# Optimization experiments

Hardware: AMD Instinct MI355X
Metric: run time of the kernel (lower is better)

## Reference

```python
import jax, jax.numpy as jnp
import numpy as np

EPS = 1e-6  # flax LayerNorm default
ROPE_BASE = 10000.0

def _ln(x, scale, bias):
    m = jnp.mean(x, axis=-1, keepdims=True)
    v = jnp.mean(jnp.square(x - m), axis=-1, keepdims=True)
    return (x - m) * jax.lax.rsqrt(v + EPS) * scale + bias

def _rope_cache(u, v, head_dim):
    # P = head_dim//2//2 pairs per axis
    P = head_dim // 4
    freqs = jnp.arange(P, dtype=jnp.float32) / (P - 1 + 1e-9)
    inv = 1.0 / ROPE_BASE ** freqs
    ang_x = jnp.einsum('nl,f->nlf', u, inv)
    ang_y = jnp.einsum('nl,f->nlf', v, inv)
    return jnp.cos(ang_x), jnp.sin(ang_x), jnp.cos(ang_y), jnp.sin(ang_y)

def _rope_apply(q, cos_x, sin_x, cos_y, sin_y):
    n, L, H, D = q.shape
    q = q.reshape(n, L, H, D // 2, 2)
    P = D // 4
    qx, qy = q[..., :P, :], q[..., P:, :]
    def rot(qp, c, s):
        c = c[:, :, None, :]
        s = s[:, :, None, :]
        x, y = qp[..., 0], qp[..., 1]
        return jnp.stack([x * c - y * s, x * s + y * c], axis=-1)
    return jnp.concatenate([rot(qx, cos_x, sin_x), rot(qy, cos_y, sin_y)], axis=-2).reshape(n, L, H, D)

def setup_inputs():
    key = jax.random.key(0)
    ks = jax.random.split(key, 12)
    N, HW, CIN = 8, 384, 3
    P, W, DPT, H, HD, MLP = 16, 768, 4, 12, 64, 3072
    s = 0.02
    return {
        'image': jax.random.normal(ks[0], (N, HW, HW, CIN), jnp.float32),
        'conv_kernel': jax.random.normal(ks[1], (P, P, CIN, W), jnp.float32) * s,
        'conv_bias': jnp.zeros((W,), jnp.float32),
        'ln1_scale': jnp.ones((DPT, W), jnp.float32),
        'ln1_bias': jnp.zeros((DPT, W), jnp.float32),
        'wq': jax.random.normal(ks[2], (DPT, W, H, HD), jnp.float32) * s,
        'bq': jnp.zeros((DPT, H, HD), jnp.float32),
        'wk': jax.random.normal(ks[3], (DPT, W, H, HD), jnp.float32) * s,
        'bk': jnp.zeros((DPT, H, HD), jnp.float32),
        'wv': jax.random.normal(ks[4], (DPT, W, H, HD), jnp.float32) * s,
        'bv': jnp.zeros((DPT, H, HD), jnp.float32),
        'wo': jax.random.normal(ks[5], (DPT, H, HD, W), jnp.float32) * s,
        'bo': jnp.zeros((DPT, W), jnp.float32),
        'ln2_scale': jnp.ones((DPT, W), jnp.float32),
        'ln2_bias': jnp.zeros((DPT, W), jnp.float32),
        'w1': jax.random.normal(ks[6], (DPT, W, MLP), jnp.float32) * s,
        'b1': jnp.zeros((DPT, MLP), jnp.float32),
        'w2': jax.random.normal(ks[7], (DPT, MLP, W), jnp.float32) * s,
        'b2': jnp.zeros((DPT, W), jnp.float32),
        'lnf_scale': jnp.ones((W,), jnp.float32),
        'lnf_bias': jnp.zeros((W,), jnp.float32),
    }

def reference(image, conv_kernel, conv_bias, ln1_scale, ln1_bias,
              wq, bq, wk, bk, wv, bv, wo, bo,
              ln2_scale, ln2_bias, w1, b1, w2, b2, lnf_scale, lnf_bias):
    patch = conv_kernel.shape[0]
    # patch-embedding conv, stride=patch, VALID padding (NHWC/HWIO)
    x = jax.lax.conv_general_dilated(
        image, conv_kernel, window_strides=(patch, patch), padding='VALID',
        dimension_numbers=('NHWC', 'HWIO', 'NHWC')) + conv_bias
    n, h, w, c = x.shape
    L = h * w
    x = x.reshape(n, L, c)

    depth, _, H, HD = wq.shape
    # RoPE 2D coordinates for square grid (default path when rope_uv is None)
    ys, xs = jnp.mgrid[:h, :w]
    u = jnp.tile(((xs.reshape(-1) + 0.5) / w)[None, :], [n, 1])
    v = jnp.tile(((ys.reshape(-1) + 0.5) / h)[None, :], [n, 1])
    cos_x, sin_x, cos_y, sin_y = _rope_cache(u, v, HD)

    scale = 1.0 / jnp.sqrt(jnp.float32(HD))
    for l in range(depth):
        y = _ln(x, ln1_scale[l], ln1_bias[l])
        q = jnp.einsum('nld,dhk->nlhk', y, wq[l]) + bq[l]
        k = jnp.einsum('nld,dhk->nlhk', y, wk[l]) + bk[l]
        vv = jnp.einsum('nld,dhk->nlhk', y, wv[l]) + bv[l]
        q = _rope_apply(q, cos_x, sin_x, cos_y, sin_y)
        k = _rope_apply(k, cos_x, sin_x, cos_y, sin_y)
        logits = jnp.einsum('nqhd,nkhd->nhqk', q, k) * scale
        attn = jax.nn.softmax(logits, axis=-1)
        o = jnp.einsum('nhqk,nkhd->nqhd', attn, vv)
        y = jnp.einsum('nqhd,hdo->nqo', o, wo[l]) + bo[l]
        x = x + y
        y = _ln(x, ln2_scale[l], ln2_bias[l])
        y = jax.nn.gelu(jnp.einsum('nld,df->nlf', y, w1[l]) + b1[l])
        y = jnp.einsum('nlf,fd->nld', y, w2[l]) + b2[l]
        x = x + y

    x = _ln(x, lnf_scale, lnf_bias)  # encoder_norm
    return jnp.mean(x, axis=1)       # gap pooling -> [n, width]
```

## Files before the change

kernel.cpp:

```cpp
#include <hip/hip_runtime.h>
#include <hip/hip_bf16.h>

typedef __hip_bfloat16 bf16;
typedef __bf16 bf16x8 __attribute__((ext_vector_type(8)));
typedef float f32x4  __attribute__((ext_vector_type(4)));

#define NBATCH 8
#define LTOK   576
#define NT     4608
#define CW     768
#define NH     12
#define HDIM   64
#define DEPTH  4
#define MLPW   3072
#define GRIDP  24
#define IMGS   384
#define QKVW   2304

static __device__ __forceinline__ unsigned bfpair(float a, float b){
    bf16 x = __float2bfloat16(a), y = __float2bfloat16(b);
    return ((unsigned)*(unsigned short*)&y << 16) | *(unsigned short*)&x;
}
static __device__ __forceinline__ float b2f(bf16 v){ return __bfloat162float(v); }

static __device__ __forceinline__ int xcd_swizzle(int orig, int nwg){
    int q = nwg >> 3, r = nwg & 7;
    int xcd = orig & 7, j = orig >> 3;
    int base = (xcd < r) ? xcd*(q+1) : r*(q+1) + (xcd-r)*q;
    return base + j;
}

static __device__ __forceinline__ void gl_lds16(const bf16* g, bf16* l){
    __builtin_amdgcn_global_load_lds(
        (const __attribute__((address_space(1))) unsigned int*)(const void*)g,
        (__attribute__((address_space(3))) unsigned int*)(void*)l, 16, 0, 0);
}

__global__ void rope_cache_kernel(float* __restrict__ rc){
    int idx = blockIdx.x*256 + threadIdx.x;
    if (idx >= LTOK*16) return;
    int l = idx >> 4, f = idx & 15;
    int py = l / GRIDP, px = l % GRIDP;
    float u = (px + 0.5f) / (float)GRIDP;
    float v = (py + 0.5f) / (float)GRIDP;
    float fr = (float)f / (15.0f + 1e-9f);
    float inv = expf(-fr * 9.210340371976184f);
    float sx, cx, sy, cy;
    sincosf(u * inv, &sx, &cx);
    sincosf(v * inv, &sy, &cy);
    rc[idx]         = cx;
    rc[idx + 9216]  = sx;
    rc[idx + 18432] = cy;
    rc[idx + 27648] = sy;
}

__global__ void patch_gather(const float* __restrict__ img, bf16* __restrict__ p){
    int idx = blockIdx.x*256 + threadIdx.x;
    int t = idx / CW, kk = idx % CW;
    int n = t / LTOK, l = t % LTOK;
    int py = l / GRIDP, px = l % GRIDP;
    int i = kk / 48, r = kk % 48, j = r / 3, c = r % 3;
    p[idx] = __float2bfloat16(img[((size_t)(n*IMGS + py*16 + i)*IMGS + px*16 + j)*3 + c]);
}

__global__ __launch_bounds__(256) void wtrans_b(const float* __restrict__ in, bf16* __restrict__ out,
                                                int K, int N, size_t inStride, size_t outStride){
    in  += blockIdx.z * inStride;
    out += blockIdx.z * outStride;
    __shared__ float t[32][33];
    const int n0 = blockIdx.x*32, k0 = blockIdx.y*32;
    const int tx = threadIdx.x & 31, ty = threadIdx.x >> 5;
    #pragma unroll
    for (int r = 0; r < 4; ++r)
        t[ty + 8*r][tx] = in[(size_t)(k0 + ty + 8*r)*N + n0 + tx];
    __syncthreads();
    #pragma unroll
    for (int r = 0; r < 4; ++r)
        out[(size_t)(n0 + ty + 8*r)*K + k0 + tx] = __float2bfloat16(t[tx][ty + 8*r]);
}

__global__ void bias_pack(const float* __restrict__ bq, const float* __restrict__ bk,
                          const float* __restrict__ bv, float* __restrict__ o){
    int idx = blockIdx.x*256 + threadIdx.x;
    int l = idx / QKVW, r = idx % QKVW;
    const float* src = (r < 768) ? (bq + l*768 + r) :
                       (r < 1536) ? (bk + l*768 + r - 768) : (bv + l*768 + r - 1536);
    o[idx] = *src;
}

static __device__ __forceinline__ float gelu_tanh(float x){
    float x3 = x*x*x;
    return 0.5f*x*(1.0f + tanhf(0.7978845608028654f*(x + 0.044715f*x3)));
}

template<int EPI, typename TC>
__global__ __launch_bounds__(256) void gemm_a(const bf16* __restrict__ A, int lda,
                                              const bf16* __restrict__ B, int ldb,
                                              const float* __restrict__ bias,
                                              TC* __restrict__ C, int ldc, int K){
    __shared__ bf16 As[2][128*64];
    __shared__ bf16 Bs[2][64*64];
    const int tid = threadIdx.x;
    const int w = tid >> 6, l = tid & 63;
    const int quad = l >> 4, lr = l & 15;
    const int wm = w & 1, wn = w >> 1;

    const int nwg = gridDim.x * gridDim.y;
    const int swz = xcd_swizzle(blockIdx.y * gridDim.x + blockIdx.x, nwg);
    const int rowT = (swz / gridDim.x) * 128;
    const int colT = (swz % gridDim.x) * 64;

    const int srow = l >> 3;
    const int schk = (l & 7) ^ (srow & 7);

    const bf16* Ap[4];
    const bf16* Bp[2];
    #pragma unroll
    for (int t = 0; t < 4; ++t)
        Ap[t] = A + (size_t)(rowT + (w*4+t)*8 + srow)*lda + schk*8;
    #pragma unroll
    for (int t = 0; t < 2; ++t)
        Bp[t] = B + (size_t)(colT + (w*2+t)*8 + srow)*ldb + schk*8;

    auto STAGE = [&](int k0, int buf){
        #pragma unroll
        for (int t = 0; t < 4; ++t) gl_lds16(Ap[t] + k0, &As[buf][(w*4+t)*512]);
        #pragma unroll
        for (int t = 0; t < 2; ++t) gl_lds16(Bp[t] + k0, &Bs[buf][(w*2+t)*512]);
    };

    f32x4 acc[4][2];
    #pragma unroll
    for (int i = 0; i < 4; ++i)
        #pragma unroll
        for (int j = 0; j < 2; ++j) acc[i][j] = (f32x4){0.f,0.f,0.f,0.f};

    const int S = K >> 6;
    STAGE(0, 0);
    if (S > 1) STAGE(64, 1);

    int cur = 0;
    for (int s = 0; s < S; ++s){
        if (s < S-1) asm volatile("s_waitcnt vmcnt(6)" ::: "memory");
        else         asm volatile("s_waitcnt vmcnt(0)" ::: "memory");
        __builtin_amdgcn_s_barrier();
        #pragma unroll
        for (int kh = 0; kh < 2; ++kh){
            bf16x8 af[4], bfr[2];
            #pragma unroll
            for (int i = 0; i < 4; ++i){
                int r = wm*64 + i*16 + lr;
                af[i] = *(const bf16x8*)(&As[cur][r*64 + (((kh*4 + quad) ^ (r & 7))*8)]);
            }
            #pragma unroll
            for (int j = 0; j < 2; ++j){
                int r = wn*32 + j*16 + lr;
                bfr[j] = *(const bf16x8*)(&Bs[cur][r*64 + (((kh*4 + quad) ^ (r & 7))*8)]);
            }
            #pragma unroll
            for (int i = 0; i < 4; ++i)
                #pragma unroll
                for (int j = 0; j < 2; ++j)
                    acc[i][j] = __builtin_amdgcn_mfma_f32_16x16x32_bf16(af[i], bfr[j], acc[i][j], 0, 0, 0);
        }
        __builtin_amdgcn_s_barrier();
        if (s + 2 < S) STAGE((s + 2)*64, cur);
        cur ^= 1;
    }

    #pragma unroll
    for (int i = 0; i < 4; ++i){
        #pragma unroll
        for (int j = 0; j < 2; ++j){
            const int row = rowT + wm*64 + i*16 + quad*4;
            const int col = colT + wn*32 + j*16 + lr;
            const float bb = bias ? bias[col] : 0.f;
            #pragma unroll
            for (int r = 0; r < 4; ++r){
                float val = acc[i][j][r] + bb;
                TC* cp = C + (size_t)(row + r)*ldc + col;
                if (EPI == 2) val = gelu_tanh(val);
                if (EPI == 1) val += *(float*)cp;
                if (EPI == 0 || EPI == 2) *(bf16*)cp = __float2bfloat16(val);
                else                      *(float*)cp = val;
            }
        }
    }
}

__global__ __launch_bounds__(256) void ln_wave(const float* __restrict__ x,
                                               const float* __restrict__ sc,
                                               const float* __restrict__ bs,
                                               bf16* __restrict__ y){
    const int tid = threadIdx.x, w = tid >> 6, l = tid & 63;
    const int t = blockIdx.x*4 + w;
    const float4* xr = (const float4*)(x + (size_t)t*CW);
    float4 a[3];
    #pragma unroll
    for (int i = 0; i < 3; ++i) a[i] = xr[l + 64*i];
    float s = 0.f;
    #pragma unroll
    for (int i = 0; i < 3; ++i) s += a[i].x + a[i].y + a[i].z + a[i].w;
    #pragma unroll
    for (int off = 1; off < 64; off <<= 1) s += __shfl_xor(s, off);
    const float m = s * (1.0f/768.0f);
    float vs = 0.f;
    #pragma unroll
    for (int i = 0; i < 3; ++i){
        float dx = a[i].x-m, dy = a[i].y-m, dz = a[i].z-m, dw = a[i].w-m;
        vs += dx*dx + dy*dy + dz*dz + dw*dw;
    }
    #pragma unroll
    for (int off = 1; off < 64; off <<= 1) vs += __shfl_xor(vs, off);
    const float rs = rsqrtf(vs*(1.0f/768.0f) + 1e-6f);
    const float4* scp = (const float4*)sc;
    const float4* bsp = (const float4*)bs;
    uint2* yr = (uint2*)(y + (size_t)t*CW);
    #pragma unroll
    for (int i = 0; i < 3; ++i){
        float4 sv = scp[l + 64*i], bv = bsp[l + 64*i];
        float r0 = (a[i].x-m)*rs*sv.x + bv.x;
        float r1 = (a[i].y-m)*rs*sv.y + bv.y;
        float r2 = (a[i].z-m)*rs*sv.z + bv.z;
        float r3 = (a[i].w-m)*rs*sv.w + bv.w;
        yr[l + 64*i] = make_uint2(bfpair(r0,r1), bfpair(r2,r3));
    }
}

__global__ void rope_qk(bf16* __restrict__ qkv, const float* __restrict__ rc){
    int idx = blockIdx.x*256 + threadIdx.x;
    int tok = idx / 768;
    int r = idx % 768;
    int rr, base;
    if (r < 384){ base = 0; rr = r; } else { base = 768; rr = r - 384; }
    int hh = rr >> 5, p = rr & 31;
    int l = tok % LTOK;
    float c, s;
    if (p < 16){ c = rc[l*16 + p];            s = rc[9216 + l*16 + p]; }
    else       { c = rc[18432 + l*16 + p-16]; s = rc[27648 + l*16 + p-16]; }
    bf16* pp = qkv + (size_t)tok*QKVW + base + hh*64 + 2*p;
    unsigned u = *(unsigned*)pp;
    bf16 lo = *(bf16*)&u; unsigned short hi16 = u >> 16; bf16 hi = *(bf16*)&hi16;
    float x = b2f(lo), y = b2f(hi);
    *(unsigned*)pp = bfpair(x*c - y*s, x*s + y*c);
}

__global__ __launch_bounds__(256) void vtrans(const bf16* __restrict__ qkv, bf16* __restrict__ vT){
    __shared__ bf16 tile[64][72];
    const int t0 = blockIdx.x*64, hI = blockIdx.y, nI = blockIdx.z;
    const size_t base = ((size_t)nI*LTOK + t0)*QKVW + 1536 + hI*64;
    const int tid = threadIdx.x;
    #pragma unroll
    for (int i = 0; i < 2; ++i){
        int g = i*256 + tid, r = g >> 3, c = g & 7;
        *(uint4*)&tile[r][c*8] = *(const uint4*)(qkv + base + (size_t)r*QKVW + c*8);
    }
    __syncthreads();
    const size_t obase = ((size_t)(nI*NH + hI)*64)*576 + t0;
    #pragma unroll
    for (int i = 0; i < 2; ++i){
        int g = i*256 + tid, d = g >> 3, c = g & 7;
        bf16 tmp[8];
        #pragma unroll
        for (int j = 0; j < 8; ++j) tmp[j] = tile[c*8 + j][d];
        *(uint4*)(vT + obase + (size_t)d*576 + c*8) = *(uint4*)tmp;
    }
}

__global__ __launch_bounds__(256) void attn_flash(const bf16* __restrict__ qkv,
                                                  const bf16* __restrict__ vT,
                                                  bf16* __restrict__ o){
    __shared__ bf16 Ks[64*72];
    __shared__ bf16 Vs[64*72];
    __shared__ bf16 Ps[64*72];
    __shared__ float alph[64];
    __shared__ float lsum[64];
    const int tid = threadIdx.x;
    const int w = tid >> 6, l = tid & 63;
    const int quad = l >> 4, lr = l & 15;

    const int nwg = gridDim.x * gridDim.y * gridDim.z;
    const int orig = (blockIdx.z * gridDim.y + blockIdx.y) * gridDim.x + blockIdx.x;
    const int swz = xcd_swizzle(orig, nwg);
    const int q0 = (swz % gridDim.x) * 64;
    const int t2 = swz / gridDim.x;
    const int hI = t2 % gridDim.y;
    const int nI = t2 / gridDim.y;

    const size_t tokBase = (size_t)nI * LTOK;
    const int off = hI * 64;
    const size_t vbase = ((size_t)(nI*NH + hI)*64)*576;

    bf16x8 qf[2];
    #pragma unroll
    for (int kh = 0; kh < 2; ++kh)
        qf[kh] = *(const bf16x8*)(qkv + (tokBase + q0 + w*16 + lr)*QKVW + off + kh*32 + quad*8);

    f32x4 oacc[4];
    #pragma unroll
    for (int j = 0; j < 4; ++j) oacc[j] = (f32x4){0.f,0.f,0.f,0.f};
    float m_run = -3.0e38f, l_run = 0.f;

    for (int ch = 0; ch < 9; ++ch){
        __syncthreads();
        #pragma unroll
        for (int i = 0; i < 2; ++i){
            int g = i*256 + tid, r = g >> 3, c = g & 7;
            *(uint4*)(Ks + r*72 + c*8) =
                *(const uint4*)(qkv + (tokBase + ch*64 + r)*QKVW + 768 + off + c*8);
        }
        #pragma unroll
        for (int i = 0; i < 2; ++i){
            int g = i*256 + tid, d = g >> 3, c = g & 7;
            *(uint4*)(Vs + d*72 + c*8) = *(const uint4*)(vT + vbase + (size_t)d*576 + ch*64 + c*8);
        }
        __syncthreads();

        f32x4 st[4];
        #pragma unroll
        for (int t = 0; t < 4; ++t){
            st[t] = (f32x4){0.f,0.f,0.f,0.f};
            #pragma unroll
            for (int kh = 0; kh < 2; ++kh){
                bf16x8 kf = *(const bf16x8*)(Ks + (t*16 + lr)*72 + kh*32 + quad*8);
                st[t] = __builtin_amdgcn_mfma_f32_16x16x32_bf16(kf, qf[kh], st[t], 0, 0, 0);
            }
        }
        float lm = -3.0e38f;
        #pragma unroll
        for (int t = 0; t < 4; ++t)
            #pragma unroll
            for (int r = 0; r < 4; ++r){
                st[t][r] *= 0.125f;
                lm = fmaxf(lm, st[t][r]);
            }
        lm = fmaxf(lm, __shfl_xor(lm, 16));
        lm = fmaxf(lm, __shfl_xor(lm, 32));
        float mn = fmaxf(m_run, lm);
        float alpha = __expf(m_run - mn);
        m_run = mn;
        float ls = 0.f;
        #pragma unroll
        for (int t = 0; t < 4; ++t)
            #pragma unroll
            for (int r = 0; r < 4; ++r){
                float p = __expf(st[t][r] - mn);
                st[t][r] = p; ls += p;
            }
        ls += __shfl_xor(ls, 16);
        ls += __shfl_xor(ls, 32);
        l_run = l_run*alpha + ls;
        if ((tid & 48) == 0) alph[w*16 + lr] = alpha;
        #pragma unroll
        for (int t = 0; t < 4; ++t)
            #pragma unroll
            for (int r = 0; r < 4; ++r)
                Ps[(w*16 + lr)*72 + t*16 + quad*4 + r] = __float2bfloat16(st[t][r]);
        float af[4];
        #pragma unroll
        for (int r = 0; r < 4; ++r) af[r] = alph[w*16 + quad*4 + r];
        #pragma unroll
        for (int j = 0; j < 4; ++j)
            #pragma unroll
            for (int r = 0; r < 4; ++r) oacc[j][r] *= af[r];
        #pragma unroll
        for (int kh = 0; kh < 2; ++kh){
            bf16x8 pf = *(const bf16x8*)(Ps + (w*16 + lr)*72 + kh*32 + quad*8);
            #pragma unroll
            for (int j = 0; j < 4; ++j){
                bf16x8 vf = *(const bf16x8*)(Vs + (j*16 + lr)*72 + kh*32 + quad*8);
                oacc[j] = __builtin_amdgcn_mfma_f32_16x16x32_bf16(pf, vf, oacc[j], 0, 0, 0);
            }
        }
    }

    if ((tid & 48) == 0) lsum[w*16 + lr] = l_run;
    float linv[4];
    #pragma unroll
    for (int r = 0; r < 4; ++r) linv[r] = 1.0f / lsum[w*16 + quad*4 + r];
    #pragma unroll
    for (int j = 0; j < 4; ++j)
        #pragma unroll
        for (int r = 0; r < 4; ++r)
            o[(tokBase + q0 + w*16 + quad*4 + r)*CW + off + j*16 + lr] =
                __float2bfloat16(oacc[j][r] * linv[r]);
}

__global__ void mean_kernel(const bf16* __restrict__ y, float* __restrict__ out){
    int c = blockIdx.x*256 + threadIdx.x;
    int n = blockIdx.y;
    float s = 0.f;
    for (int l = 0; l < LTOK; ++l) s += b2f(y[((size_t)n*LTOK + l)*CW + c]);
    out[n*CW + c] = s * (1.0f/576.0f);
}

extern "C" void kernel_launch(void* const* d_in, const int* in_sizes, int n_in,
                              void* d_out, int out_size, void* d_ws, size_t ws_size,
                              hipStream_t stream){
    const float* image = (const float*)d_in[0];
    const float* convk = (const float*)d_in[1];
    const float* convb = (const float*)d_in[2];
    const float* ln1s  = (const float*)d_in[3];
    const float* ln1b  = (const float*)d_in[4];
    const float* wq    = (const float*)d_in[5];
    const float* bq    = (const float*)d_in[6];
    const float* wk    = (const float*)d_in[7];
    const float* bk    = (const float*)d_in[8];
    const float* wv    = (const float*)d_in[9];
    const float* bv    = (const float*)d_in[10];
    const float* wo    = (const float*)d_in[11];
    const float* bo    = (const float*)d_in[12];
    const float* ln2s  = (const float*)d_in[13];
    const float* ln2b  = (const float*)d_in[14];
    const float* w1    = (const float*)d_in[15];
    const float* b1    = (const float*)d_in[16];
    const float* w2    = (const float*)d_in[17];
    const float* b2    = (const float*)d_in[18];
    const float* lnfs  = (const float*)d_in[19];
    const float* lnfb  = (const float*)d_in[20];
    float* out = (float*)d_out;

    const size_t u = (size_t)NT*CW;
    float* ws    = (float*)d_ws;
    float* ropeC = ws;
    float* bqkvA = ws + 36864;
    float* x     = bqkvA + 4*QKVW;
    bf16*  y     = (bf16*)(x + u);
    bf16*  qkv   = y + u;
    bf16*  o     = qkv + (size_t)NT*QKVW;
    bf16*  h     = o + u;
    bf16*  vT    = h + (size_t)NT*MLPW;
    bf16*  convT = vT + u;
    bf16*  wqkvT = convT + 589824;
    bf16*  woT   = wqkvT + (size_t)4*QKVW*CW;
    bf16*  w1T   = woT + (size_t)4*CW*CW;
    bf16*  w2T   = w1T + (size_t)4*CW*MLPW;

    rope_cache_kernel<<<36, 256, 0, stream>>>(ropeC);
    patch_gather<<<(NT*CW)/256, 256, 0, stream>>>(image, y);
    bias_pack<<<36, 256, 0, stream>>>(bq, bk, bv, bqkvA);
    wtrans_b<<<dim3(24,24,1), 256, 0, stream>>>(convk, convT, CW, CW, 0, 0);
    wtrans_b<<<dim3(24,24,4), 256, 0, stream>>>(wq, wqkvT,           CW, CW, (size_t)CW*CW, (size_t)QKVW*CW);
    wtrans_b<<<dim3(24,24,4), 256, 0, stream>>>(wk, wqkvT + 589824,  CW, CW, (size_t)CW*CW, (size_t)QKVW*CW);
    wtrans_b<<<dim3(24,24,4), 256, 0, stream>>>(wv, wqkvT + 1179648, CW, CW, (size_t)CW*CW, (size_t)QKVW*CW);
    wtrans_b<<<dim3(24,24,4), 256, 0, stream>>>(wo, woT,             CW, CW, (size_t)CW*CW, (size_t)CW*CW);
    wtrans_b<<<dim3(96,24,4), 256, 0, stream>>>(w1, w1T,  CW, MLPW, (size_t)CW*MLPW, (size_t)CW*MLPW);
    wtrans_b<<<dim3(24,96,4), 256, 0, stream>>>(w2, w2T, MLPW,  CW, (size_t)CW*MLPW, (size_t)CW*MLPW);

    gemm_a<3,float><<<dim3(12,36), 256, 0, stream>>>(y, CW, convT, CW, convb, x, CW, CW);

    for (int l = 0; l < DEPTH; ++l){
        ln_wave<<<NT/4, 256, 0, stream>>>(x, ln1s + l*CW, ln1b + l*CW, y);
        gemm_a<0,bf16><<<dim3(36,36), 256, 0, stream>>>(y, CW, wqkvT + (size_t)l*QKVW*CW, CW,
                                                        bqkvA + l*QKVW, qkv, QKVW, CW);
        rope_qk<<<(NT*768)/256, 256, 0, stream>>>(qkv, ropeC);
        vtrans<<<dim3(9, NH, NBATCH), 256, 0, stream>>>(qkv, vT);
        attn_flash<<<dim3(9, NH, NBATCH), 256, 0, stream>>>(qkv, vT, o);
        gemm_a<1,float><<<dim3(12,36), 256, 0, stream>>>(o, CW, woT + (size_t)l*CW*CW, CW,
                                                         bo + l*CW, x, CW, CW);
        ln_wave<<<NT/4, 256, 0, stream>>>(x, ln2s + l*CW, ln2b + l*CW, y);
        gemm_a<2,bf16><<<dim3(48,36), 256, 0, stream>>>(y, CW, w1T + (size_t)l*CW*MLPW, CW,
                                                        b1 + l*MLPW, h, MLPW, CW);
        gemm_a<1,float><<<dim3(12,36), 256, 0, stream>>>(h, MLPW, w2T + (size_t)l*CW*MLPW, MLPW,
                                                         b2 + l*CW, x, CW, MLPW);
    }
    ln_wave<<<NT/4, 256, 0, stream>>>(x, lnfs, lnfb, y);
    mean_kernel<<<dim3(3, NBATCH), 256, 0, stream>>>(y, out);
}
```

Baseline: 1.020 ms.

## Add 256x256-tile 8-wave GEMM with interleaved staging for most projections

Adds a new GEMM kernel with 512 threads and 256x256 output tiles. It interleaves the global-to-LDS staging of the next K slice with the MFMA phases and raises wave priority around the MFMA groups. The kernel is used for the patch embedding, QKV, output projection and MLP-up GEMMs, while the MLP-down GEMM stays on the old kernel. Larger tiles raise operand reuse per block, but they cut the grid to 54–216 blocks on a 256-CU device, which risks under-filling the GPU for the small-N GEMMs.

```diff
diff --git a/kernel.cpp b/kernel.cpp
--- a/kernel.cpp
+++ b/kernel.cpp
@@ -94,6 +94,157 @@
 }
 
 template<int EPI, typename TC>
+__global__ __launch_bounds__(512) void gemm8(const bf16* __restrict__ A, int lda,
+                                             const bf16* __restrict__ B, int ldb,
+                                             const float* __restrict__ bias,
+                                             TC* __restrict__ C, int ldc, int K){
+    __shared__ bf16 As[2][2][128*64];
+    __shared__ bf16 Bs[2][2][128*64];
+    const int tid = threadIdx.x;
+    const int w = tid >> 6, l = tid & 63;
+    const int quad = l >> 4, lr = l & 15;
+    const int wm = w >> 2, wn = w & 3;
+
+    const int nwg = gridDim.x * gridDim.y;
+    const int swz = xcd_swizzle(blockIdx.y * gridDim.x + blockIdx.x, nwg);
+    const int rowT = (swz / gridDim.x) * 256;
+    const int colT = (swz % gridDim.x) * 256;
+
+    const int srow = l >> 3;
+    const int schk = (l & 7) ^ (srow & 7);
+
+    const bf16 *ApH[2][2], *BpH[2][2];
+    #pragma unroll
+    for (int h = 0; h < 2; ++h)
+        #pragma unroll
+        for (int t = 0; t < 2; ++t){
+            ApH[h][t] = A + (size_t)(rowT + h*128 + (w*2+t)*8 + srow)*lda + schk*8;
+            BpH[h][t] = B + (size_t)(colT + h*128 + (w*2+t)*8 + srow)*ldb + schk*8;
+        }
+
+    auto STAGE_A = [&](int k0, int buf){
+        #pragma unroll
+        for (int h = 0; h < 2; ++h)
+            #pragma unroll
+            for (int t = 0; t < 2; ++t)
+                gl_lds16(ApH[h][t] + k0, &As[buf][h][(w*2+t)*512]);
+    };
+    auto STAGE_B = [&](int k0, int buf){
+        #pragma unroll
+        for (int h = 0; h < 2; ++h)
+            #pragma unroll
+            for (int t = 0; t < 2; ++t)
+                gl_lds16(BpH[h][t] + k0, &Bs[buf][h][(w*2+t)*512]);
+    };
+
+    f32x4 acc[8][4];
+    #pragma unroll
+    for (int i = 0; i < 8; ++i)
+        #pragma unroll
+        for (int j = 0; j < 4; ++j) acc[i][j] = (f32x4){0.f,0.f,0.f,0.f};
+
+    const int S = K >> 6;
+    STAGE_A(0, 0);
+    STAGE_B(0, 0);
+
+    int cur = 0;
+    for (int s = 0; s < S; ++s){
+        asm volatile("s_waitcnt vmcnt(0)" ::: "memory");
+        __builtin_amdgcn_s_barrier();
+        asm volatile("" ::: "memory");
+        const bf16* Ah = &As[cur][wm][0];
+        const bf16* Bh = &Bs[cur][wn >> 1][0];
+        const int bc = (wn & 1) * 64;
+        bf16x8 af[4], bfr[4];
+
+        if (s + 1 < S) STAGE_A((s+1)*64, cur^1);
+        #pragma unroll
+        for (int j = 0; j < 4; ++j){
+            int rl = bc + j*16 + lr;
+            bfr[j] = *(const bf16x8*)(Bh + rl*64 + ((quad ^ (rl & 7))*8));
+        }
+        #pragma unroll
+        for (int i = 0; i < 4; ++i){
+            int rl = i*16 + lr;
+            af[i] = *(const bf16x8*)(Ah + rl*64 + ((quad ^ (rl & 7))*8));
+        }
+        __builtin_amdgcn_s_setprio(1);
+        #pragma unroll
+        for (int i = 0; i < 4; ++i)
+            #pragma unroll
+            for (int j = 0; j < 4; ++j)
+                acc[i][j] = __builtin_amdgcn_mfma_f32_16x16x32_bf16(af[i], bfr[j], acc[i][j], 0, 0, 0);
+        __builtin_amdgcn_s_setprio(0);
+
+        if (s + 1 < S) STAGE_B((s+1)*64, cur^1);
+        #pragma unroll
+        for (int i = 0; i < 4; ++i){
+            int rl = (i+4)*16 + lr;
+            af[i] = *(const bf16x8*)(Ah + rl*64 + ((quad ^ (rl & 7))*8));
+        }
+        __builtin_amdgcn_s_setprio(1);
+        #pragma unroll
+        for (int i = 0; i < 4; ++i)
+            #pragma unroll
+            for (int j = 0; j < 4; ++j)
+                acc[i+4][j] = __builtin_amdgcn_mfma_f32_16x16x32_bf16(af[i], bfr[j], acc[i+4][j], 0, 0, 0);
+        __builtin_amdgcn_s_setprio(0);
+
+        #pragma unroll
+        for (int j = 0; j < 4; ++j){
+            int rl = bc + j*16 + lr;
+            bfr[j] = *(const bf16x8*)(Bh + rl*64 + (((4 + quad) ^ (rl & 7))*8));
+        }
+        #pragma unroll
+        for (int i = 0; i < 4; ++i){
+            int rl = i*16 + lr;
+            af[i] = *(const bf16x8*)(Ah + rl*64 + (((4 + quad) ^ (rl & 7))*8));
+        }
+        __builtin_amdgcn_s_setprio(1);
+        #pragma unroll
+        for (int i = 0; i < 4; ++i)
+            #pragma unroll
+            for (int j = 0; j < 4; ++j)
+                acc[i][j] = __builtin_amdgcn_mfma_f32_16x16x32_bf16(af[i], bfr[j], acc[i][j], 0, 0, 0);
+        __builtin_amdgcn_s_setprio(0);
+
+        #pragma unroll
+        for (int i = 0; i < 4; ++i){
+            int rl = (i+4)*16 + lr;
+            af[i] = *(const bf16x8*)(Ah + rl*64 + (((4 + quad) ^ (rl & 7))*8));
+        }
+        __builtin_amdgcn_s_setprio(1);
+        #pragma unroll
+        for (int i = 0; i < 4; ++i)
+            #pragma unroll
+            for (int j = 0; j < 4; ++j)
+                acc[i+4][j] = __builtin_amdgcn_mfma_f32_16x16x32_bf16(af[i], bfr[j], acc[i+4][j], 0, 0, 0);
+        __builtin_amdgcn_s_setprio(0);
+
+        cur ^= 1;
+    }
+
+    #pragma unroll
+    for (int i = 0; i < 8; ++i){
+        #pragma unroll
+        for (int j = 0; j < 4; ++j){
+            const int row = rowT + wm*128 + i*16 + quad*4;
+            const int col = colT + wn*64 + j*16 + lr;
+            const float bb = bias ? bias[col] : 0.f;
+            #pragma unroll
+            for (int r = 0; r < 4; ++r){
+                float val = acc[i][j][r] + bb;
+                TC* cp = C + (size_t)(row + r)*ldc + col;
+                if (EPI == 2) val = gelu_tanh(val);
+                if (EPI == 1) val += *(float*)cp;
+                if (EPI == 0 || EPI == 2) *(bf16*)cp = __float2bfloat16(val);
+                else                      *(float*)cp = val;
+            }
+        }
+    }
+}
+
+template<int EPI, typename TC>
 __global__ __launch_bounds__(256) void gemm_a(const bf16* __restrict__ A, int lda,
                                               const bf16* __restrict__ B, int ldb,
                                               const float* __restrict__ bias,
@@ -144,6 +295,7 @@
         if (s < S-1) asm volatile("s_waitcnt vmcnt(6)" ::: "memory");
         else         asm volatile("s_waitcnt vmcnt(0)" ::: "memory");
         __builtin_amdgcn_s_barrier();
+        asm volatile("" ::: "memory");
         #pragma unroll
         for (int kh = 0; kh < 2; ++kh){
             bf16x8 af[4], bfr[2];
@@ -447,20 +599,20 @@
     wtrans_b<<<dim3(96,24,4), 256, 0, stream>>>(w1, w1T,  CW, MLPW, (size_t)CW*MLPW, (size_t)CW*MLPW);
     wtrans_b<<<dim3(24,96,4), 256, 0, stream>>>(w2, w2T, MLPW,  CW, (size_t)CW*MLPW, (size_t)CW*MLPW);
 
-    gemm_a<3,float><<<dim3(12,36), 256, 0, stream>>>(y, CW, convT, CW, convb, x, CW, CW);
+    gemm8<3,float><<<dim3(3,18), 512, 0, stream>>>(y, CW, convT, CW, convb, x, CW, CW);
 
     for (int l = 0; l < DEPTH; ++l){
         ln_wave<<<NT/4, 256, 0, stream>>>(x, ln1s + l*CW, ln1b + l*CW, y);
-        gemm_a<0,bf16><<<dim3(36,36), 256, 0, stream>>>(y, CW, wqkvT + (size_t)l*QKVW*CW, CW,
-                                                        bqkvA + l*QKVW, qkv, QKVW, CW);
+        gemm8<0,bf16><<<dim3(9,18), 512, 0, stream>>>(y, CW, wqkvT + (size_t)l*QKVW*CW, CW,
+                                                      bqkvA + l*QKVW, qkv, QKVW, CW);
         rope_qk<<<(NT*768)/256, 256, 0, stream>>>(qkv, ropeC);
         vtrans<<<dim3(9, NH, NBATCH), 256, 0, stream>>>(qkv, vT);
         attn_flash<<<dim3(9, NH, NBATCH), 256, 0, stream>>>(qkv, vT, o);
-        gemm_a<1,float><<<dim3(12,36), 256, 0, stream>>>(o, CW, woT + (size_t)l*CW*CW, CW,
-                                                         bo + l*CW, x, CW, CW);
+        gemm8<1,float><<<dim3(3,18), 512, 0, stream>>>(o, CW, woT + (size_t)l*CW*CW, CW,
+                                                       bo + l*CW, x, CW, CW);
         ln_wave<<<NT/4, 256, 0, stream>>>(x, ln2s + l*CW, ln2b + l*CW, y);
-        gemm_a<2,bf16><<<dim3(48,36), 256, 0, stream>>>(y, CW, w1T + (size_t)l*CW*MLPW, CW,
-                                                        b1 + l*MLPW, h, MLPW, CW);
+        gemm8<2,bf16><<<dim3(12,18), 512, 0, stream>>>(y, CW, w1T + (size_t)l*CW*MLPW, CW,
+                                                       b1 + l*MLPW, h, MLPW, CW);
         gemm_a<1,float><<<dim3(12,36), 256, 0, stream>>>(h, MLPW, w2T + (size_t)l*CW*MLPW, MLPW,
                                                          b2 + l*CW, x, CW, MLPW);
     }
```

New measurement: 1.226 ms. 20.3% more time.

## Fuse RoPE into QKV GEMM epilogue, drop V transpose kernel, unroll k-loop by two

Applied to the files above, without the earlier changes.

Applies the rotary embedding to Q and K inside the QKV GEMM epilogue, pairing adjacent columns with a lane shuffle, so the separate rope_qk pass over the QKV buffer goes away. The V transpose kernel is removed and attention now transposes V into shared memory while staging each chunk. The GEMM main loop is unrolled by two with fixed buffer indices. The cost is scattered 2-byte LDS writes in attention, which may cause bank conflicts, and the unrolled loop assumes an even number of k-steps.

```diff
diff --git a/kernel.cpp b/kernel.cpp
--- a/kernel.cpp
+++ b/kernel.cpp
@@ -97,7 +97,8 @@
 __global__ __launch_bounds__(256) void gemm_a(const bf16* __restrict__ A, int lda,
                                               const bf16* __restrict__ B, int ldb,
                                               const float* __restrict__ bias,
-                                              TC* __restrict__ C, int ldc, int K){
+                                              TC* __restrict__ C, int ldc, int K,
+                                              const float* __restrict__ rc){
     __shared__ bf16 As[2][128*64];
     __shared__ bf16 Bs[2][64*64];
     const int tid = threadIdx.x;
@@ -135,27 +136,19 @@
         #pragma unroll
         for (int j = 0; j < 2; ++j) acc[i][j] = (f32x4){0.f,0.f,0.f,0.f};
 
-    const int S = K >> 6;
-    STAGE(0, 0);
-    if (S > 1) STAGE(64, 1);
-
-    int cur = 0;
-    for (int s = 0; s < S; ++s){
-        if (s < S-1) asm volatile("s_waitcnt vmcnt(6)" ::: "memory");
-        else         asm volatile("s_waitcnt vmcnt(0)" ::: "memory");
-        __builtin_amdgcn_s_barrier();
+    auto KCOMP = [&](const bf16* __restrict__ Ac, const bf16* __restrict__ Bc){
         #pragma unroll
         for (int kh = 0; kh < 2; ++kh){
             bf16x8 af[4], bfr[2];
             #pragma unroll
             for (int i = 0; i < 4; ++i){
                 int r = wm*64 + i*16 + lr;
-                af[i] = *(const bf16x8*)(&As[cur][r*64 + (((kh*4 + quad) ^ (r & 7))*8)]);
+                af[i] = *(const bf16x8*)(Ac + r*64 + (((kh*4 + quad) ^ (r & 7))*8));
             }
             #pragma unroll
             for (int j = 0; j < 2; ++j){
                 int r = wn*32 + j*16 + lr;
-                bfr[j] = *(const bf16x8*)(&Bs[cur][r*64 + (((kh*4 + quad) ^ (r & 7))*8)]);
+                bfr[j] = *(const bf16x8*)(Bc + r*64 + (((kh*4 + quad) ^ (r & 7))*8));
             }
             #pragma unroll
             for (int i = 0; i < 4; ++i)
@@ -163,9 +156,26 @@
                 for (int j = 0; j < 2; ++j)
                     acc[i][j] = __builtin_amdgcn_mfma_f32_16x16x32_bf16(af[i], bfr[j], acc[i][j], 0, 0, 0);
         }
+    };
+
+    const int S = K >> 6;
+    STAGE(0, 0);
+    STAGE(64, 1);
+
+    for (int s = 0; s < S; s += 2){
+        asm volatile("s_waitcnt vmcnt(6)" ::: "memory");
         __builtin_amdgcn_s_barrier();
-        if (s + 2 < S) STAGE((s + 2)*64, cur);
-        cur ^= 1;
+        asm volatile("" ::: "memory");
+        KCOMP(&As[0][0], &Bs[0][0]);
+        __builtin_amdgcn_s_barrier();
+        if (s + 2 < S) STAGE((s + 2)*64, 0);
+        if (s + 2 < S) asm volatile("s_waitcnt vmcnt(6)" ::: "memory");
+        else           asm volatile("s_waitcnt vmcnt(0)" ::: "memory");
+        __builtin_amdgcn_s_barrier();
+        asm volatile("" ::: "memory");
+        KCOMP(&As[1][0], &Bs[1][0]);
+        __builtin_amdgcn_s_barrier();
+        if (s + 3 < S) STAGE((s + 3)*64, 1);
     }
 
     #pragma unroll
@@ -175,14 +185,38 @@
             const int row = rowT + wm*64 + i*16 + quad*4;
             const int col = colT + wn*32 + j*16 + lr;
             const float bb = bias ? bias[col] : 0.f;
-            #pragma unroll
-            for (int r = 0; r < 4; ++r){
-                float val = acc[i][j][r] + bb;
-                TC* cp = C + (size_t)(row + r)*ldc + col;
-                if (EPI == 2) val = gelu_tanh(val);
-                if (EPI == 1) val += *(float*)cp;
-                if (EPI == 0 || EPI == 2) *(bf16*)cp = __float2bfloat16(val);
-                else                      *(float*)cp = val;
+            if (EPI == 5){
+                const int hcol = col & 63;
+                const int p = hcol >> 1;
+                const bool isv = (col >= 1536);
+                const bool isY = (p >= 16);
+                const int f = p & 15;
+                const int cOff = isY ? 18432 : 0;
+                const int sOff = isY ? 27648 : 9216;
+                #pragma unroll
+                for (int r = 0; r < 4; ++r){
+                    float val = acc[i][j][r] + bb;
+                    float other = __shfl_xor(val, 1);
+                    float outv = val;
+                    if (!isv){
+                        const int tok = (row + r) % LTOK;
+                        const float cc = rc[cOff + tok*16 + f];
+                        const float ss = rc[sOff + tok*16 + f];
+                        outv = ((col & 1) == 0) ? val*cc - other*ss
+                                                : other*ss + val*cc;
+                    }
+                    *(bf16*)(C + (size_t)(row + r)*ldc + col) = __float2bfloat16(outv);
+                }
+            } else {
+                #pragma unroll
+                for (int r = 0; r < 4; ++r){
+                    float val = acc[i][j][r] + bb;
+                    TC* cp = C + (size_t)(row + r)*ldc + col;
+                    if (EPI == 2) val = gelu_tanh(val);
+                    if (EPI == 1) val += *(float*)cp;
+                    if (EPI == 0 || EPI == 2) *(bf16*)cp = __float2bfloat16(val);
+                    else                      *(float*)cp = val;
+                }
             }
         }
     }
@@ -227,48 +261,7 @@
     }
 }
 
-__global__ void rope_qk(bf16* __restrict__ qkv, const float* __restrict__ rc){
-    int idx = blockIdx.x*256 + threadIdx.x;
-    int tok = idx / 768;
-    int r = idx % 768;
-    int rr, base;
-    if (r < 384){ base = 0; rr = r; } else { base = 768; rr = r - 384; }
-    int hh = rr >> 5, p = rr & 31;
-    int l = tok % LTOK;
-    float c, s;
-    if (p < 16){ c = rc[l*16 + p];            s = rc[9216 + l*16 + p]; }
-    else       { c = rc[18432 + l*16 + p-16]; s = rc[27648 + l*16 + p-16]; }
-    bf16* pp = qkv + (size_t)tok*QKVW + base + hh*64 + 2*p;
-    unsigned u = *(unsigned*)pp;
-    bf16 lo = *(bf16*)&u; unsigned short hi16 = u >> 16; bf16 hi = *(bf16*)&hi16;
-    float x = b2f(lo), y = b2f(hi);
-    *(unsigned*)pp = bfpair(x*c - y*s, x*s + y*c);
-}
-
-__global__ __launch_bounds__(256) void vtrans(const bf16* __restrict__ qkv, bf16* __restrict__ vT){
-    __shared__ bf16 tile[64][72];
-    const int t0 = blockIdx.x*64, hI = blockIdx.y, nI = blockIdx.z;
-    const size_t base = ((size_t)nI*LTOK + t0)*QKVW + 1536 + hI*64;
-    const int tid = threadIdx.x;
-    #pragma unroll
-    for (int i = 0; i < 2; ++i){
-        int g = i*256 + tid, r = g >> 3, c = g & 7;
-        *(uint4*)&tile[r][c*8] = *(const uint4*)(qkv + base + (size_t)r*QKVW + c*8);
-    }
-    __syncthreads();
-    const size_t obase = ((size_t)(nI*NH + hI)*64)*576 + t0;
-    #pragma unroll
-    for (int i = 0; i < 2; ++i){
-        int g = i*256 + tid, d = g >> 3, c = g & 7;
-        bf16 tmp[8];
-        #pragma unroll
-        for (int j = 0; j < 8; ++j) tmp[j] = tile[c*8 + j][d];
-        *(uint4*)(vT + obase + (size_t)d*576 + c*8) = *(uint4*)tmp;
-    }
-}
-
 __global__ __launch_bounds__(256) void attn_flash(const bf16* __restrict__ qkv,
-                                                  const bf16* __restrict__ vT,
                                                   bf16* __restrict__ o){
     __shared__ bf16 Ks[64*72];
     __shared__ bf16 Vs[64*72];
@@ -289,7 +282,6 @@
 
     const size_t tokBase = (size_t)nI * LTOK;
     const int off = hI * 64;
-    const size_t vbase = ((size_t)(nI*NH + hI)*64)*576;
 
     bf16x8 qf[2];
     #pragma unroll
@@ -311,8 +303,11 @@
         }
         #pragma unroll
         for (int i = 0; i < 2; ++i){
-            int g = i*256 + tid, d = g >> 3, c = g & 7;
-            *(uint4*)(Vs + d*72 + c*8) = *(const uint4*)(vT + vbase + (size_t)d*576 + ch*64 + c*8);
+            int g = i*256 + tid, r = g >> 3, c = g & 7;
+            uint4 tmp4 = *(const uint4*)(qkv + (tokBase + ch*64 + r)*QKVW + 1536 + off + c*8);
+            const bf16* t8 = (const bf16*)&tmp4;
+            #pragma unroll
+            for (int jj = 0; jj < 8; ++jj) Vs[(c*8 + jj)*72 + r] = t8[jj];
         }
         __syncthreads();
 
@@ -447,22 +442,20 @@
     wtrans_b<<<dim3(96,24,4), 256, 0, stream>>>(w1, w1T,  CW, MLPW, (size_t)CW*MLPW, (size_t)CW*MLPW);
     wtrans_b<<<dim3(24,96,4), 256, 0, stream>>>(w2, w2T, MLPW,  CW, (size_t)CW*MLPW, (size_t)CW*MLPW);
 
-    gemm_a<3,float><<<dim3(12,36), 256, 0, stream>>>(y, CW, convT, CW, convb, x, CW, CW);
+    gemm_a<3,float><<<dim3(12,36), 256, 0, stream>>>(y, CW, convT, CW, convb, x, CW, CW, nullptr);
 
     for (int l = 0; l < DEPTH; ++l){
         ln_wave<<<NT/4, 256, 0, stream>>>(x, ln1s + l*CW, ln1b + l*CW, y);
-        gemm_a<0,bf16><<<dim3(36,36), 256, 0, stream>>>(y, CW, wqkvT + (size_t)l*QKVW*CW, CW,
-                                                        bqkvA + l*QKVW, qkv, QKVW, CW);
-        rope_qk<<<(NT*768)/256, 256, 0, stream>>>(qkv, ropeC);
-        vtrans<<<dim3(9, NH, NBATCH), 256, 0, stream>>>(qkv, vT);
-        attn_flash<<<dim3(9, NH, NBATCH), 256, 0, stream>>>(qkv, vT, o);
+        gemm_a<5,bf16><<<dim3(36,36), 256, 0, stream>>>(y, CW, wqkvT + (size_t)l*QKVW*CW, CW,
+                                                        bqkvA + l*QKVW, qkv, QKVW, CW, ropeC);
+        attn_flash<<<dim3(9, NH, NBATCH), 256, 0, stream>>>(qkv, o);
         gemm_a<1,float><<<dim3(12,36), 256, 0, stream>>>(o, CW, woT + (size_t)l*CW*CW, CW,
-                                                         bo + l*CW, x, CW, CW);
+                                                         bo + l*CW, x, CW, CW, nullptr);
         ln_wave<<<NT/4, 256, 0, stream>>>(x, ln2s + l*CW, ln2b + l*CW, y);
         gemm_a<2,bf16><<<dim3(48,36), 256, 0, stream>>>(y, CW, w1T + (size_t)l*CW*MLPW, CW,
-                                                        b1 + l*MLPW, h, MLPW, CW);
+                                                        b1 + l*MLPW, h, MLPW, CW, nullptr);
         gemm_a<1,float><<<dim3(12,36), 256, 0, stream>>>(h, MLPW, w2T + (size_t)l*CW*MLPW, MLPW,
-                                                         b2 + l*CW, x, CW, MLPW);
+                                                         b2 + l*CW, x, CW, MLPW, nullptr);
     }
     ln_wave<<<NT/4, 256, 0, stream>>>(x, lnfs, lnfb, y);
     mean_kernel<<<dim3(3, NBATCH), 256, 0, stream>>>(y, out);
```

New measurement: 1.066 ms. +4.6%, slower.
